# Performance work log

Measured on AMD Instinct MI355X. Metric: run time of the kernel, lower is better.

The kernel has to match this reference:

```python
import jax, jax.numpy as jnp
import numpy as np

B = 65536      # batch
D = 512        # embedding_dim
H = 256        # hidden_size
NB = 6         # num_branch


def setup_inputs() -> dict:
    key = jax.random.key(0)
    ks = jax.random.split(key, 12)
    sc = 0.05
    s = lambda k, shape: (jax.random.normal(k, shape, jnp.float32) * sc)
    inp = {}
    inp["embedding"] = jax.random.normal(ks[0], (B, D), jnp.float32)
    inp["speed"] = jax.random.normal(ks[1], (B,), jnp.float32)
    inp["command"] = jax.random.randint(ks[2], (B,), 1, NB + 1)  # values 1..6
    # speed_in: Linear(1,H) -> ReLU -> Linear(H,D)   (weights stored [in,out])
    inp["sw1"] = s(ks[3], (1, H)); inp["sb1"] = jnp.zeros((H,), jnp.float32)
    inp["sw2"] = s(ks[4], (H, D)); inp["sb2"] = jnp.zeros((D,), jnp.float32)
    # 6 branch MLPs, stacked along leading axis: D->H->H->3, sigmoid
    inp["bw1"] = s(ks[5], (NB, D, H)); inp["bb1"] = jnp.zeros((NB, H), jnp.float32)
    inp["bw2"] = s(ks[6], (NB, H, H)); inp["bb2"] = jnp.zeros((NB, H), jnp.float32)
    inp["bw3"] = s(ks[7], (NB, H, 3)); inp["bb3"] = jnp.zeros((NB, 3), jnp.float32)
    # speed_out: D->H->H->1
    inp["ow1"] = s(ks[8], (D, H)); inp["ob1"] = jnp.zeros((H,), jnp.float32)
    inp["ow2"] = s(ks[9], (H, H)); inp["ob2"] = jnp.zeros((H,), jnp.float32)
    inp["ow3"] = s(ks[10], (H, 1)); inp["ob3"] = jnp.zeros((1,), jnp.float32)
    return inp


def reference(embedding, speed, command,
              sw1, sb1, sw2, sb2,
              bw1, bb1, bw2, bb2, bw3, bb3,
              ow1, ob1, ow2, ob2, ow3, ob3):
    # embedding += speed_in(speed.unsqueeze(1))
    sh = jax.nn.relu(speed[:, None] @ sw1 + sb1)           # [B,H]
    emb = embedding + (sh @ sw2 + sb2)                      # [B,D]

    # all 6 branches computed densely (as in the original), then masked
    h = jax.nn.relu(jnp.einsum('bd,ndh->nbh', emb, bw1) + bb1[:, None, :])   # [NB,B,H]
    h = jax.nn.relu(jnp.einsum('nbh,nhk->nbk', h, bw2) + bb2[:, None, :])    # [NB,B,H]
    br = jax.nn.sigmoid(jnp.einsum('nbh,nho->nbo', h, bw3) + bb3[:, None, :])  # [NB,B,3]

    # mask: branch i selected where i == command - 1
    mask = (jnp.arange(NB)[:, None] == (command - 1)[None, :]).astype(br.dtype)  # [NB,B]
    control_pred = jnp.sum(br * mask[:, :, None], axis=0)   # [B,3]

    # speed_out head
    t = jax.nn.relu(emb @ ow1 + ob1)
    t = jax.nn.relu(t @ ow2 + ob2)
    speed_pred = t @ ow3 + ob3                               # [B,1]
    return control_pred, speed_pred
```

## Files before the change

### kernel.cpp

```cpp
#include <hip/hip_runtime.h>
#include <math.h>


#define B_ 65536
#define D_ 512
#define H_ 256

typedef float  f32x4   __attribute__((ext_vector_type(4)));
typedef __bf16 bf16x8  __attribute__((ext_vector_type(8)));
typedef __bf16 bf16x4  __attribute__((ext_vector_type(4)));
typedef float  float4v __attribute__((ext_vector_type(4)));

#define OFF_PERM     256
#define OFF_PACK     262400
#define WS_NEEDED    3277056

#define PKO_SW2   0u
#define PKO_BW1   131072u
#define PKO_BW2   917504u
#define PKO_OW1   1310720u
#define PKO_OW2   1441792u

#define PITCH_E 520


__global__ __launch_bounds__(256) void k_count(const int* __restrict__ command,
                                               int* __restrict__ counts) {
    __shared__ int lh[6];
    int t = threadIdx.x;
    if (t < 6) lh[t] = 0;
    __syncthreads();
    int i = blockIdx.x * 256 + t;
    int4 v = ((const int4*)command)[i];
    int a[4] = {v.x, v.y, v.z, v.w};
    #pragma unroll
    for (int j = 0; j < 4; ++j) {
        int c = min(max(a[j] - 1, 0), 5);
        atomicAdd(&lh[c], 1);
    }
    __syncthreads();
    if (t < 6) atomicAdd(&counts[t], lh[t]);
}


__global__ __launch_bounds__(256) void k_prepB(const int* __restrict__ command,
                                               const int* __restrict__ counts,
                                               int* __restrict__ cursor2,
                                               int* __restrict__ perm,
                                               const float* __restrict__ sw2,
                                               const float* __restrict__ bw1,
                                               const float* __restrict__ bw2,
                                               const float* __restrict__ ow1,
                                               const float* __restrict__ ow2,
                                               __bf16* __restrict__ PK) {
    int t = threadIdx.x;
    if (blockIdx.x < 256) {
        __shared__ int lh[6], lbase[6];
        if (t < 6) lh[t] = 0;
        __syncthreads();
        int i = blockIdx.x * 256 + t;
        int c = command[i] - 1; c = min(max(c, 0), 5);
        int rank = atomicAdd(&lh[c], 1);
        __syncthreads();
        if (t < 6) {
            int base = 0;
            #pragma unroll
            for (int k = 0; k < 6; ++k) base += (k < t) ? counts[k] : 0;
            lbase[t] = base + atomicAdd(&cursor2[t], lh[t]);
        }
        __syncthreads();
        perm[lbase[c] + rank] = i;
        return;
    }
    int b = blockIdx.x - 256;
    const float* src; int srcN, colOff; unsigned dstOff; int tt;
    if (b < 64)       { int s = b >> 5;        tt = b & 31;  src = sw2;                          srcN = 512; colOff = s * 256; dstOff = PKO_SW2 + s * 65536u; }
    else if (b < 448) { int i = b - 64;  int c = i >> 6; tt = i & 63; src = bw1 + (size_t)c * 512 * 256; srcN = 256; colOff = 0; dstOff = PKO_BW1 + c * 131072u; }
    else if (b < 640) { int i = b - 448; int c = i >> 5; tt = i & 31; src = bw2 + (size_t)c * 256 * 256; srcN = 256; colOff = 0; dstOff = PKO_BW2 + c * 65536u; }
    else if (b < 704) { tt = b - 640; src = ow1; srcN = 256; colOff = 0; dstOff = PKO_OW1; }
    else              { tt = b - 704; src = ow2; srcN = 256; colOff = 0; dstOff = PKO_OW2; }
    int kc = tt >> 2, nt = tt & 3;
    int k0 = kc * 32, n0 = nt * 64;

    __shared__ __bf16 T[64][34];
    #pragma unroll
    for (int p = 0; p < 2; ++p) {
        int idx = p * 256 + t;
        int k = idx >> 4, n4 = idx & 15;
        float4v v = *(const float4v*)(src + (size_t)(k0 + k) * srcN + colOff + n0 + n4 * 4);
        T[n4 * 4 + 0][k] = (__bf16)v[0];
        T[n4 * 4 + 1][k] = (__bf16)v[1];
        T[n4 * 4 + 2][k] = (__bf16)v[2];
        T[n4 * 4 + 3][k] = (__bf16)v[3];
    }
    __syncthreads();
    int n = t >> 2, seg = t & 3;
    bf16x8 v;
    #pragma unroll
    for (int j = 0; j < 8; ++j) v[j] = T[n][seg * 8 + j];
    *(bf16x8*)(PK + dstOff + ((unsigned)(kc * 256 + n0 + n) * 32u + seg * 8u)) = v;
}


__global__ __launch_bounds__(512, 4) void k_fused(
    const float* __restrict__ embedding, const float* __restrict__ speed,
    const int*   __restrict__ command,
    const float* __restrict__ sw1, const float* __restrict__ sb1,
    const float* __restrict__ sb2,
    const float* __restrict__ bb1, const float* __restrict__ bb2,
    const float* __restrict__ bw3, const float* __restrict__ bb3,
    const float* __restrict__ ob1, const float* __restrict__ ob2,
    const float* __restrict__ ow3, const float* __restrict__ ob3,
    const int* __restrict__ perm, const __bf16* __restrict__ PK,
    float* __restrict__ out)
{
    __shared__ __bf16 s_x[64 * PITCH_E];
    __shared__ float  s_head[64][4];
    __shared__ int    s_row[64];
    __shared__ int    s_cmd[64];
    __shared__ float  s_spd[64];

    const int tid = threadIdx.x;
    const int w = tid >> 6, lane = tid & 63;
    const int lm = lane & 15, kg = lane >> 4;
    const int R0 = blockIdx.x * 64;

    if (tid < 64) {
        int r = perm[R0 + tid];
        s_row[tid] = r;
        int c = command[r] - 1; c = min(max(c, 0), 5);
        s_cmd[tid] = c;
        s_spd[tid] = speed[r];
        s_head[tid][0] = 0.f; s_head[tid][1] = 0.f; s_head[tid][2] = 0.f; s_head[tid][3] = 0.f;
    }
    __syncthreads();

    #pragma unroll
    for (int it = 0; it < 16; ++it) {
        int idx = it * 512 + tid;
        int row = idx >> 7, c4 = idx & 127;
        float4v v = __builtin_nontemporal_load(
            (const float4v*)(embedding + (size_t)s_row[row] * D_ + c4 * 4));
        bf16x4 pv;
        pv[0] = (__bf16)v[0]; pv[1] = (__bf16)v[1];
        pv[2] = (__bf16)v[2]; pv[3] = (__bf16)v[3];
        *(bf16x4*)(s_x + row * PITCH_E + c4 * 4) = pv;
    }
    __syncthreads();

    const int cmin = s_cmd[0], cmax = s_cmd[63];

    {
        float spd[4];
        #pragma unroll
        for (int nt = 0; nt < 4; ++nt) spd[nt] = s_spd[nt * 16 + lm];
        const unsigned slice = (unsigned)(w >> 2) * 65536u;
        const int mbase = (w & 3) * 64;
        f32x4 dacc[4][4];
        #pragma unroll
        for (int mt = 0; mt < 4; ++mt)
            #pragma unroll
            for (int nt = 0; nt < 4; ++nt) dacc[mt][nt] = f32x4{0.f, 0.f, 0.f, 0.f};
        #pragma unroll 4
        for (int ks = 0; ks < 8; ++ks) {
            const int k0 = ks * 32 + kg * 8;
            float4v w0 = *(const float4v*)(sw1 + k0);
            float4v w1 = *(const float4v*)(sw1 + k0 + 4);
            float4v c0 = *(const float4v*)(sb1 + k0);
            float4v c1 = *(const float4v*)(sb1 + k0 + 4);
            bf16x8 bns[4];
            #pragma unroll
            for (int nt = 0; nt < 4; ++nt)
                #pragma unroll
                for (int j = 0; j < 4; ++j) {
                    bns[nt][j]     = (__bf16)fmaxf(spd[nt] * w0[j] + c0[j], 0.f);
                    bns[nt][j + 4] = (__bf16)fmaxf(spd[nt] * w1[j] + c1[j], 0.f);
                }
            const __bf16* ap = PK + PKO_SW2 + slice + (size_t)ks * 8192
                             + (size_t)(mbase + lm) * 32 + kg * 8;
            __builtin_amdgcn_s_setprio(1);
            #pragma unroll
            for (int mt = 0; mt < 4; ++mt) {
                bf16x8 av = *(const bf16x8*)(ap + mt * 512);
                #pragma unroll
                for (int nt = 0; nt < 4; ++nt)
                    dacc[mt][nt] = __builtin_amdgcn_mfma_f32_16x16x32_bf16(av, bns[nt], dacc[mt][nt], 0, 0, 0);
            }
            __builtin_amdgcn_s_setprio(0);
        }
        #pragma unroll
        for (int mt = 0; mt < 4; ++mt) {
            int colb = w * 64 + mt * 16 + kg * 4;
            float4v sbv = *(const float4v*)(sb2 + colb);
            #pragma unroll
            for (int nt = 0; nt < 4; ++nt) {
                int row = nt * 16 + lm;
                bf16x4* p = (bf16x4*)(s_x + row * PITCH_E + colb);
                bf16x4 old = *p;
                bf16x4 nv;
                #pragma unroll
                for (int g = 0; g < 4; ++g)
                    nv[g] = (__bf16)(dacc[mt][nt][g] + sbv[g] + (float)old[g]);
                *p = nv;
            }
        }
    }
    __syncthreads();

    const bool roleB = (w < 4);
    const int colbase = (w & 3) * 64;
    const unsigned laneoffB = (unsigned)(colbase + lm) * 32u + kg * 8u;
    const __bf16* aXbase = s_x + lm * PITCH_E + kg * 8;

    bf16x4 res[4][4];
    if (roleB) {
        for (int c = cmin; c <= cmax; ++c) {
            const __bf16* bb = PK + PKO_BW1 + (unsigned)c * 131072u + laneoffB;
            f32x4 ah[4][4];
            #pragma unroll
            for (int mt = 0; mt < 4; ++mt)
                #pragma unroll
                for (int ct = 0; ct < 4; ++ct) ah[mt][ct] = f32x4{0.f, 0.f, 0.f, 0.f};
            #pragma unroll 4
            for (int ks = 0; ks < 16; ++ks) {
                bf16x8 a[4];
                #pragma unroll
                for (int mt = 0; mt < 4; ++mt)
                    a[mt] = *(const bf16x8*)(aXbase + mt * 16 * PITCH_E + ks * 32);
                __builtin_amdgcn_s_setprio(1);
                #pragma unroll
                for (int ct = 0; ct < 4; ++ct) {
                    bf16x8 bv = *(const bf16x8*)(bb + (size_t)ks * 8192 + ct * 512);
                    #pragma unroll
                    for (int mt = 0; mt < 4; ++mt)
                        ah[mt][ct] = __builtin_amdgcn_mfma_f32_16x16x32_bf16(a[mt], bv, ah[mt][ct], 0, 0, 0);
                }
                __builtin_amdgcn_s_setprio(0);
            }
            #pragma unroll
            for (int ct = 0; ct < 4; ++ct) {
                int col = colbase + ct * 16 + lm;
                float b = bb1[c * H_ + col];
                #pragma unroll
                for (int mt = 0; mt < 4; ++mt)
                    #pragma unroll
                    for (int g = 0; g < 4; ++g)
                        if (s_cmd[mt * 16 + kg * 4 + g] == c)
                            res[mt][ct][g] = (__bf16)fmaxf(ah[mt][ct][g] + b, 0.f);
            }
        }
    } else {
        const __bf16* bb = PK + PKO_OW1 + laneoffB;
        f32x4 ta[4][4];
        #pragma unroll
        for (int mt = 0; mt < 4; ++mt)
            #pragma unroll
            for (int ct = 0; ct < 4; ++ct) ta[mt][ct] = f32x4{0.f, 0.f, 0.f, 0.f};
        #pragma unroll 4
        for (int ks = 0; ks < 16; ++ks) {
            bf16x8 a[4];
            #pragma unroll
            for (int mt = 0; mt < 4; ++mt)
                a[mt] = *(const bf16x8*)(aXbase + mt * 16 * PITCH_E + ks * 32);
            __builtin_amdgcn_s_setprio(1);
            #pragma unroll
            for (int ct = 0; ct < 4; ++ct) {
                bf16x8 bv = *(const bf16x8*)(bb + (size_t)ks * 8192 + ct * 512);
                #pragma unroll
                for (int mt = 0; mt < 4; ++mt)
                    ta[mt][ct] = __builtin_amdgcn_mfma_f32_16x16x32_bf16(a[mt], bv, ta[mt][ct], 0, 0, 0);
            }
            __builtin_amdgcn_s_setprio(0);
        }
        #pragma unroll
        for (int ct = 0; ct < 4; ++ct) {
            int col = colbase + ct * 16 + lm;
            float b = ob1[col];
            #pragma unroll
            for (int mt = 0; mt < 4; ++mt)
                #pragma unroll
                for (int g = 0; g < 4; ++g)
                    res[mt][ct][g] = (__bf16)fmaxf(ta[mt][ct][g] + b, 0.f);
        }
    }
    __syncthreads();

    {
        const int colW = (roleB ? 0 : 256) + colbase;
        #pragma unroll
        for (int ct = 0; ct < 4; ++ct) {
            int col = colW + ct * 16 + lm;
            #pragma unroll
            for (int mt = 0; mt < 4; ++mt)
                #pragma unroll
                for (int g = 0; g < 4; ++g)
                    s_x[(mt * 16 + kg * 4 + g) * PITCH_E + col] = res[mt][ct][g];
        }
    }
    __syncthreads();

    const __bf16* aHbase = s_x + lm * PITCH_E + (roleB ? 0 : 256) + kg * 8;
    if (roleB) {
        for (int c = cmin; c <= cmax; ++c) {
            const __bf16* bb = PK + PKO_BW2 + (unsigned)c * 65536u + laneoffB;
            #pragma unroll
            for (int rh = 0; rh < 2; ++rh) {
                f32x4 hh[2][4];
                #pragma unroll
                for (int mt = 0; mt < 2; ++mt)
                    #pragma unroll
                    for (int ct = 0; ct < 4; ++ct) hh[mt][ct] = f32x4{0.f, 0.f, 0.f, 0.f};
                #pragma unroll 4
                for (int ks = 0; ks < 8; ++ks) {
                    bf16x8 a0 = *(const bf16x8*)(aHbase + (rh * 2 + 0) * 16 * PITCH_E + ks * 32);
                    bf16x8 a1 = *(const bf16x8*)(aHbase + (rh * 2 + 1) * 16 * PITCH_E + ks * 32);
                    __builtin_amdgcn_s_setprio(1);
                    #pragma unroll
                    for (int ct = 0; ct < 4; ++ct) {
                        bf16x8 bv = *(const bf16x8*)(bb + (size_t)ks * 8192 + ct * 512);
                        hh[0][ct] = __builtin_amdgcn_mfma_f32_16x16x32_bf16(a0, bv, hh[0][ct], 0, 0, 0);
                        hh[1][ct] = __builtin_amdgcn_mfma_f32_16x16x32_bf16(a1, bv, hh[1][ct], 0, 0, 0);
                    }
                    __builtin_amdgcn_s_setprio(0);
                }
                float ph[2][4][3];
                #pragma unroll
                for (int mt = 0; mt < 2; ++mt)
                    #pragma unroll
                    for (int g = 0; g < 4; ++g) { ph[mt][g][0] = 0.f; ph[mt][g][1] = 0.f; ph[mt][g][2] = 0.f; }
                #pragma unroll
                for (int ct = 0; ct < 4; ++ct) {
                    int col = colbase + ct * 16 + lm;
                    float b  = bb2[c * H_ + col];
                    float w0 = bw3[(c * H_ + col) * 3 + 0];
                    float w1 = bw3[(c * H_ + col) * 3 + 1];
                    float w2 = bw3[(c * H_ + col) * 3 + 2];
                    #pragma unroll
                    for (int mt = 0; mt < 2; ++mt)
                        #pragma unroll
                        for (int g = 0; g < 4; ++g) {
                            float h = fmaxf(hh[mt][ct][g] + b, 0.f);
                            ph[mt][g][0] += h * w0; ph[mt][g][1] += h * w1; ph[mt][g][2] += h * w2;
                        }
                }
                #pragma unroll
                for (int mt = 0; mt < 2; ++mt)
                    #pragma unroll
                    for (int g = 0; g < 4; ++g)
                        #pragma unroll
                        for (int o = 0; o < 3; ++o) {
                            float v = ph[mt][g][o];
                            v += __shfl_xor(v, 1); v += __shfl_xor(v, 2);
                            v += __shfl_xor(v, 4); v += __shfl_xor(v, 8);
                            ph[mt][g][o] = v;
                        }
                if (lm == 0) {
                    #pragma unroll
                    for (int mt = 0; mt < 2; ++mt)
                        #pragma unroll
                        for (int g = 0; g < 4; ++g) {
                            int row = (rh * 2 + mt) * 16 + kg * 4 + g;
                            if (s_cmd[row] == c) {
                                atomicAdd(&s_head[row][0], ph[mt][g][0]);
                                atomicAdd(&s_head[row][1], ph[mt][g][1]);
                                atomicAdd(&s_head[row][2], ph[mt][g][2]);
                            }
                        }
                }
            }
        }
    } else {
        float sp[4][4];
        #pragma unroll
        for (int mt = 0; mt < 4; ++mt)
            #pragma unroll
            for (int g = 0; g < 4; ++g) sp[mt][g] = 0.f;
        const __bf16* bb = PK + PKO_OW2 + laneoffB;
        #pragma unroll
        for (int rh = 0; rh < 2; ++rh) {
            f32x4 hh[2][4];
            #pragma unroll
            for (int mt = 0; mt < 2; ++mt)
                #pragma unroll
                for (int ct = 0; ct < 4; ++ct) hh[mt][ct] = f32x4{0.f, 0.f, 0.f, 0.f};
            #pragma unroll 4
            for (int ks = 0; ks < 8; ++ks) {
                bf16x8 a0 = *(const bf16x8*)(aHbase + (rh * 2 + 0) * 16 * PITCH_E + ks * 32);
                bf16x8 a1 = *(const bf16x8*)(aHbase + (rh * 2 + 1) * 16 * PITCH_E + ks * 32);
                __builtin_amdgcn_s_setprio(1);
                #pragma unroll
                for (int ct = 0; ct < 4; ++ct) {
                    bf16x8 bv = *(const bf16x8*)(bb + (size_t)ks * 8192 + ct * 512);
                    hh[0][ct] = __builtin_amdgcn_mfma_f32_16x16x32_bf16(a0, bv, hh[0][ct], 0, 0, 0);
                    hh[1][ct] = __builtin_amdgcn_mfma_f32_16x16x32_bf16(a1, bv, hh[1][ct], 0, 0, 0);
                }
                __builtin_amdgcn_s_setprio(0);
            }
            #pragma unroll
            for (int ct = 0; ct < 4; ++ct) {
                int col = colbase + ct * 16 + lm;
                float b = ob2[col], wv = ow3[col];
                #pragma unroll
                for (int mt = 0; mt < 2; ++mt)
                    #pragma unroll
                    for (int g = 0; g < 4; ++g)
                        sp[rh * 2 + mt][g] += fmaxf(hh[mt][ct][g] + b, 0.f) * wv;
            }
        }
        #pragma unroll
        for (int mt = 0; mt < 4; ++mt)
            #pragma unroll
            for (int g = 0; g < 4; ++g) {
                float v = sp[mt][g];
                v += __shfl_xor(v, 1); v += __shfl_xor(v, 2);
                v += __shfl_xor(v, 4); v += __shfl_xor(v, 8);
                if (lm == 0) atomicAdd(&s_head[mt * 16 + kg * 4 + g][3], v);
            }
    }
    __syncthreads();

    if (tid < 64) {
        int r = s_row[tid], c = s_cmd[tid];
        #pragma unroll
        for (int o = 0; o < 3; ++o) {
            float x = s_head[tid][o] + bb3[c * 3 + o];
            __builtin_nontemporal_store(1.f / (1.f + __expf(-x)), &out[(size_t)r * 3 + o]);
        }
        __builtin_nontemporal_store(s_head[tid][3] + ob3[0], &out[(size_t)3 * B_ + r]);
    }
}


__global__ __launch_bounds__(256) void cilrs_slow(
    const float* __restrict__ embedding, const float* __restrict__ speed,
    const int* __restrict__ command,
    const float* __restrict__ sw1, const float* __restrict__ sb1,
    const float* __restrict__ sw2, const float* __restrict__ sb2,
    const float* __restrict__ bw1, const float* __restrict__ bb1,
    const float* __restrict__ bw2, const float* __restrict__ bb2,
    const float* __restrict__ bw3, const float* __restrict__ bb3,
    const float* __restrict__ ow1, const float* __restrict__ ob1,
    const float* __restrict__ ow2, const float* __restrict__ ob2,
    const float* __restrict__ ow3, const float* __restrict__ ob3,
    float* __restrict__ out)
{
    const int row = blockIdx.x;
    const int j   = threadIdx.x;
    __shared__ float sh[H_];
    __shared__ float emb[D_];
    __shared__ float h1[H_];
    __shared__ float h2[H_];
    const float spd = speed[row];
    { float v = spd * sw1[j] + sb1[j]; sh[j] = v > 0.f ? v : 0.f; }
    __syncthreads();
    {
        float a0 = 0.f, a1 = 0.f;
        for (int h = 0; h < H_; ++h) {
            const float s = sh[h];
            a0 += s * sw2[h * D_ + j];
            a1 += s * sw2[h * D_ + j + 256];
        }
        emb[j]       = embedding[(size_t)row * D_ + j]       + a0 + sb2[j];
        emb[j + 256] = embedding[(size_t)row * D_ + j + 256] + a1 + sb2[j + 256];
    }
    __syncthreads();
    const int n = command[row] - 1;
    {
        const float* wp = bw1 + (size_t)n * D_ * H_;
        float a = 0.f;
        for (int d = 0; d < D_; ++d) a += emb[d] * wp[d * H_ + j];
        a += bb1[n * H_ + j];
        h1[j] = a > 0.f ? a : 0.f;
    }
    __syncthreads();
    {
        const float* wp = bw2 + (size_t)n * H_ * H_;
        float a = 0.f;
        for (int h = 0; h < H_; ++h) a += h1[h] * wp[h * H_ + j];
        a += bb2[n * H_ + j];
        h2[j] = a > 0.f ? a : 0.f;
    }
    __syncthreads();
    {
        float a = 0.f;
        for (int d = 0; d < D_; ++d) a += emb[d] * ow1[d * H_ + j];
        a += ob1[j];
        sh[j] = a > 0.f ? a : 0.f;
    }
    __syncthreads();
    {
        float a = 0.f;
        for (int h = 0; h < H_; ++h) a += sh[h] * ow2[h * H_ + j];
        a += ob2[j];
        h1[j] = a > 0.f ? a : 0.f;
    }
    __syncthreads();
    if (j < 3) {
        const float* wp = bw3 + (size_t)n * H_ * 3;
        float a = 0.f;
        for (int h = 0; h < H_; ++h) a += h2[h] * wp[h * 3 + j];
        a += bb3[n * 3 + j];
        out[(size_t)row * 3 + j] = 1.f / (1.f + expf(-a));
    } else if (j == 3) {
        float a = 0.f;
        for (int h = 0; h < H_; ++h) a += h1[h] * ow3[h];
        a += ob3[0];
        out[(size_t)B_ * 3 + row] = a;
    }
}


extern "C" void kernel_launch(void* const* d_in, const int* in_sizes, int n_in,
                              void* d_out, int out_size, void* d_ws, size_t ws_size,
                              hipStream_t stream) {
    const float* embedding = (const float*)d_in[0];
    const float* speed     = (const float*)d_in[1];
    const int*   command   = (const int*)  d_in[2];
    const float* sw1 = (const float*)d_in[3];
    const float* sb1 = (const float*)d_in[4];
    const float* sw2 = (const float*)d_in[5];
    const float* sb2 = (const float*)d_in[6];
    const float* bw1 = (const float*)d_in[7];
    const float* bb1 = (const float*)d_in[8];
    const float* bw2 = (const float*)d_in[9];
    const float* bb2 = (const float*)d_in[10];
    const float* bw3 = (const float*)d_in[11];
    const float* bb3 = (const float*)d_in[12];
    const float* ow1 = (const float*)d_in[13];
    const float* ob1 = (const float*)d_in[14];
    const float* ow2 = (const float*)d_in[15];
    const float* ob2 = (const float*)d_in[16];
    const float* ow3 = (const float*)d_in[17];
    const float* ob3 = (const float*)d_in[18];
    float* out = (float*)d_out;

    if (ws_size < (size_t)WS_NEEDED) {
        cilrs_slow<<<B_, 256, 0, stream>>>(embedding, speed, command,
                                           sw1, sb1, sw2, sb2,
                                           bw1, bb1, bw2, bb2, bw3, bb3,
                                           ow1, ob1, ow2, ob2, ow3, ob3, out);
        return;
    }

    char* ws = (char*)d_ws;
    int*    counts  = (int*)    ws;
    int*    cursor2 = (int*)   (ws + 24);
    int*    perm    = (int*)   (ws + OFF_PERM);
    __bf16* PK      = (__bf16*)(ws + OFF_PACK);

    hipMemsetAsync(ws, 0, 64, stream);
    k_count<<<64, 256, 0, stream>>>(command, counts);
    k_prepB<<<992, 256, 0, stream>>>(command, counts, cursor2, perm,
                                     sw2, bw1, bw2, ow1, ow2, PK);
    k_fused<<<B_ / 64, 512, 0, stream>>>(embedding, speed, command,
                                         sw1, sb1, sb2,
                                         bb1, bb2, bw3, bb3,
                                         ob1, ob2, ow3, ob3,
                                         perm, PK, out);
}
```

Baseline: 351.5 us.

## Double rows per block to 128 and reshape per-wave MFMA tiles

The fused kernel now handles 128 rows per block with 1024 threads instead of 64 rows with 512. Each wave computes 32 output columns over all 128 rows rather than 64 columns over 64 rows, and every layer's MFMA loops are reshaped to match. Each weight fragment fetched from global memory now feeds twice as many rows, which targets L2 weight traffic. In exchange, the LDS footprint roughly doubles, likely allowing only one block per CU. A 128-row block may also span more branch commands, which adds redundant branch work.

```diff
diff --git a/kernel.cpp b/kernel.cpp
--- a/kernel.cpp
+++ b/kernel.cpp
@@ -102,7 +102,7 @@
 }
 
 
-__global__ __launch_bounds__(512, 4) void k_fused(
+__global__ __launch_bounds__(1024, 4) void k_fused(
     const float* __restrict__ embedding, const float* __restrict__ speed,
     const int*   __restrict__ command,
     const float* __restrict__ sw1, const float* __restrict__ sb1,
@@ -114,18 +114,18 @@
     const int* __restrict__ perm, const __bf16* __restrict__ PK,
     float* __restrict__ out)
 {
-    __shared__ __bf16 s_x[64 * PITCH_E];
-    __shared__ float  s_head[64][4];
-    __shared__ int    s_row[64];
-    __shared__ int    s_cmd[64];
-    __shared__ float  s_spd[64];
+    __shared__ __bf16 s_x[128 * PITCH_E];
+    __shared__ float  s_head[128][4];
+    __shared__ int    s_row[128];
+    __shared__ int    s_cmd[128];
+    __shared__ float  s_spd[128];
 
     const int tid = threadIdx.x;
     const int w = tid >> 6, lane = tid & 63;
     const int lm = lane & 15, kg = lane >> 4;
-    const int R0 = blockIdx.x * 64;
-
-    if (tid < 64) {
+    const int R0 = blockIdx.x * 128;
+
+    if (tid < 128) {
         int r = perm[R0 + tid];
         s_row[tid] = r;
         int c = command[r] - 1; c = min(max(c, 0), 5);
@@ -137,7 +137,7 @@
 
     #pragma unroll
     for (int it = 0; it < 16; ++it) {
-        int idx = it * 512 + tid;
+        int idx = it * 1024 + tid;
         int row = idx >> 7, c4 = idx & 127;
         float4v v = __builtin_nontemporal_load(
             (const float4v*)(embedding + (size_t)s_row[row] * D_ + c4 * 4));
@@ -148,101 +148,105 @@
     }
     __syncthreads();
 
-    const int cmin = s_cmd[0], cmax = s_cmd[63];
-
-    {
-        float spd[4];
-        #pragma unroll
-        for (int nt = 0; nt < 4; ++nt) spd[nt] = s_spd[nt * 16 + lm];
-        const unsigned slice = (unsigned)(w >> 2) * 65536u;
-        const int mbase = (w & 3) * 64;
-        f32x4 dacc[4][4];
-        #pragma unroll
-        for (int mt = 0; mt < 4; ++mt)
-            #pragma unroll
-            for (int nt = 0; nt < 4; ++nt) dacc[mt][nt] = f32x4{0.f, 0.f, 0.f, 0.f};
-        #pragma unroll 4
-        for (int ks = 0; ks < 8; ++ks) {
-            const int k0 = ks * 32 + kg * 8;
-            float4v w0 = *(const float4v*)(sw1 + k0);
-            float4v w1 = *(const float4v*)(sw1 + k0 + 4);
-            float4v c0 = *(const float4v*)(sb1 + k0);
-            float4v c1 = *(const float4v*)(sb1 + k0 + 4);
-            bf16x8 bns[4];
-            #pragma unroll
-            for (int nt = 0; nt < 4; ++nt)
-                #pragma unroll
-                for (int j = 0; j < 4; ++j) {
-                    bns[nt][j]     = (__bf16)fmaxf(spd[nt] * w0[j] + c0[j], 0.f);
-                    bns[nt][j + 4] = (__bf16)fmaxf(spd[nt] * w1[j] + c1[j], 0.f);
-                }
-            const __bf16* ap = PK + PKO_SW2 + slice + (size_t)ks * 8192
-                             + (size_t)(mbase + lm) * 32 + kg * 8;
-            __builtin_amdgcn_s_setprio(1);
-            #pragma unroll
-            for (int mt = 0; mt < 4; ++mt) {
-                bf16x8 av = *(const bf16x8*)(ap + mt * 512);
+    const int cmin = s_cmd[0], cmax = s_cmd[127];
+
+    {
+        const unsigned slice = (unsigned)(w >> 3) * 65536u;
+        const int mbase = (w & 7) * 32;
+        #pragma unroll
+        for (int p = 0; p < 2; ++p) {
+            float spd[4];
+            #pragma unroll
+            for (int nt = 0; nt < 4; ++nt) spd[nt] = s_spd[p * 64 + nt * 16 + lm];
+            f32x4 dacc[2][4];
+            #pragma unroll
+            for (int mt = 0; mt < 2; ++mt)
+                #pragma unroll
+                for (int nt = 0; nt < 4; ++nt) dacc[mt][nt] = f32x4{0.f, 0.f, 0.f, 0.f};
+            #pragma unroll 2
+            for (int ks = 0; ks < 8; ++ks) {
+                const int k0 = ks * 32 + kg * 8;
+                float4v w0 = *(const float4v*)(sw1 + k0);
+                float4v w1 = *(const float4v*)(sw1 + k0 + 4);
+                float4v c0 = *(const float4v*)(sb1 + k0);
+                float4v c1 = *(const float4v*)(sb1 + k0 + 4);
+                bf16x8 bns[4];
                 #pragma unroll
                 for (int nt = 0; nt < 4; ++nt)
-                    dacc[mt][nt] = __builtin_amdgcn_mfma_f32_16x16x32_bf16(av, bns[nt], dacc[mt][nt], 0, 0, 0);
-            }
-            __builtin_amdgcn_s_setprio(0);
-        }
-        #pragma unroll
-        for (int mt = 0; mt < 4; ++mt) {
-            int colb = w * 64 + mt * 16 + kg * 4;
-            float4v sbv = *(const float4v*)(sb2 + colb);
-            #pragma unroll
-            for (int nt = 0; nt < 4; ++nt) {
-                int row = nt * 16 + lm;
-                bf16x4* p = (bf16x4*)(s_x + row * PITCH_E + colb);
-                bf16x4 old = *p;
-                bf16x4 nv;
-                #pragma unroll
-                for (int g = 0; g < 4; ++g)
-                    nv[g] = (__bf16)(dacc[mt][nt][g] + sbv[g] + (float)old[g]);
-                *p = nv;
-            }
-        }
-    }
-    __syncthreads();
-
-    const bool roleB = (w < 4);
-    const int colbase = (w & 3) * 64;
+                    #pragma unroll
+                    for (int j = 0; j < 4; ++j) {
+                        bns[nt][j]     = (__bf16)fmaxf(spd[nt] * w0[j] + c0[j], 0.f);
+                        bns[nt][j + 4] = (__bf16)fmaxf(spd[nt] * w1[j] + c1[j], 0.f);
+                    }
+                const __bf16* ap = PK + PKO_SW2 + slice + (size_t)ks * 8192
+                                 + (size_t)(mbase + lm) * 32 + kg * 8;
+                __builtin_amdgcn_s_setprio(1);
+                #pragma unroll
+                for (int mt = 0; mt < 2; ++mt) {
+                    bf16x8 av = *(const bf16x8*)(ap + mt * 512);
+                    #pragma unroll
+                    for (int nt = 0; nt < 4; ++nt)
+                        dacc[mt][nt] = __builtin_amdgcn_mfma_f32_16x16x32_bf16(av, bns[nt], dacc[mt][nt], 0, 0, 0);
+                }
+                __builtin_amdgcn_s_setprio(0);
+            }
+            #pragma unroll
+            for (int mt = 0; mt < 2; ++mt) {
+                int colb = w * 32 + mt * 16 + kg * 4;
+                float4v sbv = *(const float4v*)(sb2 + colb);
+                #pragma unroll
+                for (int nt = 0; nt < 4; ++nt) {
+                    int row = p * 64 + nt * 16 + lm;
+                    bf16x4* ptr = (bf16x4*)(s_x + row * PITCH_E + colb);
+                    bf16x4 old = *ptr;
+                    bf16x4 nv;
+                    #pragma unroll
+                    for (int g = 0; g < 4; ++g)
+                        nv[g] = (__bf16)(dacc[mt][nt][g] + sbv[g] + (float)old[g]);
+                    *ptr = nv;
+                }
+            }
+        }
+    }
+    __syncthreads();
+
+    const bool roleB = (w < 8);
+    const int colbase = (w & 7) * 32;
     const unsigned laneoffB = (unsigned)(colbase + lm) * 32u + kg * 8u;
     const __bf16* aXbase = s_x + lm * PITCH_E + kg * 8;
 
-    bf16x4 res[4][4];
+    bf16x4 res[8][2];
     if (roleB) {
         for (int c = cmin; c <= cmax; ++c) {
             const __bf16* bb = PK + PKO_BW1 + (unsigned)c * 131072u + laneoffB;
-            f32x4 ah[4][4];
-            #pragma unroll
-            for (int mt = 0; mt < 4; ++mt)
-                #pragma unroll
-                for (int ct = 0; ct < 4; ++ct) ah[mt][ct] = f32x4{0.f, 0.f, 0.f, 0.f};
-            #pragma unroll 4
+            f32x4 ah[8][2];
+            #pragma unroll
+            for (int mt = 0; mt < 8; ++mt) {
+                ah[mt][0] = f32x4{0.f, 0.f, 0.f, 0.f};
+                ah[mt][1] = f32x4{0.f, 0.f, 0.f, 0.f};
+            }
+            #pragma unroll 2
             for (int ks = 0; ks < 16; ++ks) {
-                bf16x8 a[4];
-                #pragma unroll
-                for (int mt = 0; mt < 4; ++mt)
-                    a[mt] = *(const bf16x8*)(aXbase + mt * 16 * PITCH_E + ks * 32);
+                bf16x8 bv0 = *(const bf16x8*)(bb + (size_t)ks * 8192);
+                bf16x8 bv1 = *(const bf16x8*)(bb + (size_t)ks * 8192 + 512);
                 __builtin_amdgcn_s_setprio(1);
                 #pragma unroll
-                for (int ct = 0; ct < 4; ++ct) {
-                    bf16x8 bv = *(const bf16x8*)(bb + (size_t)ks * 8192 + ct * 512);
-                    #pragma unroll
-                    for (int mt = 0; mt < 4; ++mt)
-                        ah[mt][ct] = __builtin_amdgcn_mfma_f32_16x16x32_bf16(a[mt], bv, ah[mt][ct], 0, 0, 0);
+                for (int mp = 0; mp < 4; ++mp) {
+                    bf16x8 a0 = *(const bf16x8*)(aXbase + (2 * mp + 0) * 16 * PITCH_E + ks * 32);
+                    bf16x8 a1 = *(const bf16x8*)(aXbase + (2 * mp + 1) * 16 * PITCH_E + ks * 32);
+                    ah[2 * mp + 0][0] = __builtin_amdgcn_mfma_f32_16x16x32_bf16(a0, bv0, ah[2 * mp + 0][0], 0, 0, 0);
+                    ah[2 * mp + 0][1] = __builtin_amdgcn_mfma_f32_16x16x32_bf16(a0, bv1, ah[2 * mp + 0][1], 0, 0, 0);
+                    ah[2 * mp + 1][0] = __builtin_amdgcn_mfma_f32_16x16x32_bf16(a1, bv0, ah[2 * mp + 1][0], 0, 0, 0);
+                    ah[2 * mp + 1][1] = __builtin_amdgcn_mfma_f32_16x16x32_bf16(a1, bv1, ah[2 * mp + 1][1], 0, 0, 0);
                 }
                 __builtin_amdgcn_s_setprio(0);
             }
             #pragma unroll
-            for (int ct = 0; ct < 4; ++ct) {
+            for (int ct = 0; ct < 2; ++ct) {
                 int col = colbase + ct * 16 + lm;
                 float b = bb1[c * H_ + col];
                 #pragma unroll
-                for (int mt = 0; mt < 4; ++mt)
+                for (int mt = 0; mt < 8; ++mt)
                     #pragma unroll
                     for (int g = 0; g < 4; ++g)
                         if (s_cmd[mt * 16 + kg * 4 + g] == c)
@@ -251,33 +255,34 @@
         }
     } else {
         const __bf16* bb = PK + PKO_OW1 + laneoffB;
-        f32x4 ta[4][4];
-        #pragma unroll
-        for (int mt = 0; mt < 4; ++mt)
-            #pragma unroll
-            for (int ct = 0; ct < 4; ++ct) ta[mt][ct] = f32x4{0.f, 0.f, 0.f, 0.f};
-        #pragma unroll 4
+        f32x4 ta[8][2];
+        #pragma unroll
+        for (int mt = 0; mt < 8; ++mt) {
+            ta[mt][0] = f32x4{0.f, 0.f, 0.f, 0.f};
+            ta[mt][1] = f32x4{0.f, 0.f, 0.f, 0.f};
+        }
+        #pragma unroll 2
         for (int ks = 0; ks < 16; ++ks) {
-            bf16x8 a[4];
-            #pragma unroll
-            for (int mt = 0; mt < 4; ++mt)
-                a[mt] = *(const bf16x8*)(aXbase + mt * 16 * PITCH_E + ks * 32);
+            bf16x8 bv0 = *(const bf16x8*)(bb + (size_t)ks * 8192);
+            bf16x8 bv1 = *(const bf16x8*)(bb + (size_t)ks * 8192 + 512);
             __builtin_amdgcn_s_setprio(1);
             #pragma unroll
-            for (int ct = 0; ct < 4; ++ct) {
-                bf16x8 bv = *(const bf16x8*)(bb + (size_t)ks * 8192 + ct * 512);
-                #pragma unroll
-                for (int mt = 0; mt < 4; ++mt)
-                    ta[mt][ct] = __builtin_amdgcn_mfma_f32_16x16x32_bf16(a[mt], bv, ta[mt][ct], 0, 0, 0);
+            for (int mp = 0; mp < 4; ++mp) {
+                bf16x8 a0 = *(const bf16x8*)(aXbase + (2 * mp + 0) * 16 * PITCH_E + ks * 32);
+                bf16x8 a1 = *(const bf16x8*)(aXbase + (2 * mp + 1) * 16 * PITCH_E + ks * 32);
+                ta[2 * mp + 0][0] = __builtin_amdgcn_mfma_f32_16x16x32_bf16(a0, bv0, ta[2 * mp + 0][0], 0, 0, 0);
+                ta[2 * mp + 0][1] = __builtin_amdgcn_mfma_f32_16x16x32_bf16(a0, bv1, ta[2 * mp + 0][1], 0, 0, 0);
+                ta[2 * mp + 1][0] = __builtin_amdgcn_mfma_f32_16x16x32_bf16(a1, bv0, ta[2 * mp + 1][0], 0, 0, 0);
+                ta[2 * mp + 1][1] = __builtin_amdgcn_mfma_f32_16x16x32_bf16(a1, bv1, ta[2 * mp + 1][1], 0, 0, 0);
             }
             __builtin_amdgcn_s_setprio(0);
         }
         #pragma unroll
-        for (int ct = 0; ct < 4; ++ct) {
+        for (int ct = 0; ct < 2; ++ct) {
             int col = colbase + ct * 16 + lm;
             float b = ob1[col];
             #pragma unroll
-            for (int mt = 0; mt < 4; ++mt)
+            for (int mt = 0; mt < 8; ++mt)
                 #pragma unroll
                 for (int g = 0; g < 4; ++g)
                     res[mt][ct][g] = (__bf16)fmaxf(ta[mt][ct][g] + b, 0.f);
@@ -288,10 +293,10 @@
     {
         const int colW = (roleB ? 0 : 256) + colbase;
         #pragma unroll
-        for (int ct = 0; ct < 4; ++ct) {
+        for (int ct = 0; ct < 2; ++ct) {
             int col = colW + ct * 16 + lm;
             #pragma unroll
-            for (int mt = 0; mt < 4; ++mt)
+            for (int mt = 0; mt < 8; ++mt)
                 #pragma unroll
                 for (int g = 0; g < 4; ++g)
                     s_x[(mt * 16 + kg * 4 + g) * PITCH_E + col] = res[mt][ct][g];
@@ -305,38 +310,39 @@
             const __bf16* bb = PK + PKO_BW2 + (unsigned)c * 65536u + laneoffB;
             #pragma unroll
             for (int rh = 0; rh < 2; ++rh) {
-                f32x4 hh[2][4];
-                #pragma unroll
-                for (int mt = 0; mt < 2; ++mt)
-                    #pragma unroll
-                    for (int ct = 0; ct < 4; ++ct) hh[mt][ct] = f32x4{0.f, 0.f, 0.f, 0.f};
-                #pragma unroll 4
+                f32x4 hh[4][2];
+                #pragma unroll
+                for (int mt = 0; mt < 4; ++mt) {
+                    hh[mt][0] = f32x4{0.f, 0.f, 0.f, 0.f};
+                    hh[mt][1] = f32x4{0.f, 0.f, 0.f, 0.f};
+                }
+                #pragma unroll 2
                 for (int ks = 0; ks < 8; ++ks) {
-                    bf16x8 a0 = *(const bf16x8*)(aHbase + (rh * 2 + 0) * 16 * PITCH_E + ks * 32);
-                    bf16x8 a1 = *(const bf16x8*)(aHbase + (rh * 2 + 1) * 16 * PITCH_E + ks * 32);
+                    bf16x8 bv0 = *(const bf16x8*)(bb + (size_t)ks * 8192);
+                    bf16x8 bv1 = *(const bf16x8*)(bb + (size_t)ks * 8192 + 512);
                     __builtin_amdgcn_s_setprio(1);
                     #pragma unroll
-                    for (int ct = 0; ct < 4; ++ct) {
-                        bf16x8 bv = *(const bf16x8*)(bb + (size_t)ks * 8192 + ct * 512);
-                        hh[0][ct] = __builtin_amdgcn_mfma_f32_16x16x32_bf16(a0, bv, hh[0][ct], 0, 0, 0);
-                        hh[1][ct] = __builtin_amdgcn_mfma_f32_16x16x32_bf16(a1, bv, hh[1][ct], 0, 0, 0);
+                    for (int mt = 0; mt < 4; ++mt) {
+                        bf16x8 a = *(const bf16x8*)(aHbase + (rh * 4 + mt) * 16 * PITCH_E + ks * 32);
+                        hh[mt][0] = __builtin_amdgcn_mfma_f32_16x16x32_bf16(a, bv0, hh[mt][0], 0, 0, 0);
+                        hh[mt][1] = __builtin_amdgcn_mfma_f32_16x16x32_bf16(a, bv1, hh[mt][1], 0, 0, 0);
                     }
                     __builtin_amdgcn_s_setprio(0);
                 }
-                float ph[2][4][3];
-                #pragma unroll
-                for (int mt = 0; mt < 2; ++mt)
+                float ph[4][4][3];
+                #pragma unroll
+                for (int mt = 0; mt < 4; ++mt)
                     #pragma unroll
                     for (int g = 0; g < 4; ++g) { ph[mt][g][0] = 0.f; ph[mt][g][1] = 0.f; ph[mt][g][2] = 0.f; }
                 #pragma unroll
-                for (int ct = 0; ct < 4; ++ct) {
+                for (int ct = 0; ct < 2; ++ct) {
                     int col = colbase + ct * 16 + lm;
                     float b  = bb2[c * H_ + col];
                     float w0 = bw3[(c * H_ + col) * 3 + 0];
                     float w1 = bw3[(c * H_ + col) * 3 + 1];
                     float w2 = bw3[(c * H_ + col) * 3 + 2];
                     #pragma unroll
-                    for (int mt = 0; mt < 2; ++mt)
+                    for (int mt = 0; mt < 4; ++mt)
                         #pragma unroll
                         for (int g = 0; g < 4; ++g) {
                             float h = fmaxf(hh[mt][ct][g] + b, 0.f);
@@ -344,7 +350,7 @@
                         }
                 }
                 #pragma unroll
-                for (int mt = 0; mt < 2; ++mt)
+                for (int mt = 0; mt < 4; ++mt)
                     #pragma unroll
                     for (int g = 0; g < 4; ++g)
                         #pragma unroll
@@ -356,10 +362,10 @@
                         }
                 if (lm == 0) {
                     #pragma unroll
-                    for (int mt = 0; mt < 2; ++mt)
+                    for (int mt = 0; mt < 4; ++mt)
                         #pragma unroll
                         for (int g = 0; g < 4; ++g) {
-                            int row = (rh * 2 + mt) * 16 + kg * 4 + g;
+                            int row = (rh * 4 + mt) * 16 + kg * 4 + g;
                             if (s_cmd[row] == c) {
                                 atomicAdd(&s_head[row][0], ph[mt][g][0]);
                                 atomicAdd(&s_head[row][1], ph[mt][g][1]);
@@ -370,45 +376,46 @@
             }
         }
     } else {
-        float sp[4][4];
-        #pragma unroll
-        for (int mt = 0; mt < 4; ++mt)
+        float sp[8][4];
+        #pragma unroll
+        for (int mt = 0; mt < 8; ++mt)
             #pragma unroll
             for (int g = 0; g < 4; ++g) sp[mt][g] = 0.f;
         const __bf16* bb = PK + PKO_OW2 + laneoffB;
         #pragma unroll
         for (int rh = 0; rh < 2; ++rh) {
-            f32x4 hh[2][4];
-            #pragma unroll
-            for (int mt = 0; mt < 2; ++mt)
-                #pragma unroll
-                for (int ct = 0; ct < 4; ++ct) hh[mt][ct] = f32x4{0.f, 0.f, 0.f, 0.f};
-            #pragma unroll 4
+            f32x4 hh[4][2];
+            #pragma unroll
+            for (int mt = 0; mt < 4; ++mt) {
+                hh[mt][0] = f32x4{0.f, 0.f, 0.f, 0.f};
+                hh[mt][1] = f32x4{0.f, 0.f, 0.f, 0.f};
+            }
+            #pragma unroll 2
             for (int ks = 0; ks < 8; ++ks) {
-                bf16x8 a0 = *(const bf16x8*)(aHbase + (rh * 2 + 0) * 16 * PITCH_E + ks * 32);
-                bf16x8 a1 = *(const bf16x8*)(aHbase + (rh * 2 + 1) * 16 * PITCH_E + ks * 32);
+                bf16x8 bv0 = *(const bf16x8*)(bb + (size_t)ks * 8192);
+                bf16x8 bv1 = *(const bf16x8*)(bb + (size_t)ks * 8192 + 512);
                 __builtin_amdgcn_s_setprio(1);
                 #pragma unroll
-                for (int ct = 0; ct < 4; ++ct) {
-                    bf16x8 bv = *(const bf16x8*)(bb + (size_t)ks * 8192 + ct * 512);
-                    hh[0][ct] = __builtin_amdgcn_mfma_f32_16x16x32_bf16(a0, bv, hh[0][ct], 0, 0, 0);
-                    hh[1][ct] = __builtin_amdgcn_mfma_f32_16x16x32_bf16(a1, bv, hh[1][ct], 0, 0, 0);
+                for (int mt = 0; mt < 4; ++mt) {
+                    bf16x8 a = *(const bf16x8*)(aHbase + (rh * 4 + mt) * 16 * PITCH_E + ks * 32);
+                    hh[mt][0] = __builtin_amdgcn_mfma_f32_16x16x32_bf16(a, bv0, hh[mt][0], 0, 0, 0);
+                    hh[mt][1] = __builtin_amdgcn_mfma_f32_16x16x32_bf16(a, bv1, hh[mt][1], 0, 0, 0);
                 }
                 __builtin_amdgcn_s_setprio(0);
             }
             #pragma unroll
-            for (int ct = 0; ct < 4; ++ct) {
+            for (int ct = 0; ct < 2; ++ct) {
                 int col = colbase + ct * 16 + lm;
                 float b = ob2[col], wv = ow3[col];
                 #pragma unroll
-                for (int mt = 0; mt < 2; ++mt)
+                for (int mt = 0; mt < 4; ++mt)
                     #pragma unroll
                     for (int g = 0; g < 4; ++g)
-                        sp[rh * 2 + mt][g] += fmaxf(hh[mt][ct][g] + b, 0.f) * wv;
-            }
-        }
-        #pragma unroll
-        for (int mt = 0; mt < 4; ++mt)
+                        sp[rh * 4 + mt][g] += fmaxf(hh[mt][ct][g] + b, 0.f) * wv;
+            }
+        }
+        #pragma unroll
+        for (int mt = 0; mt < 8; ++mt)
             #pragma unroll
             for (int g = 0; g < 4; ++g) {
                 float v = sp[mt][g];
@@ -419,7 +426,7 @@
     }
     __syncthreads();
 
-    if (tid < 64) {
+    if (tid < 128) {
         int r = s_row[tid], c = s_cmd[tid];
         #pragma unroll
         for (int o = 0; o < 3; ++o) {
@@ -552,9 +559,9 @@
     k_count<<<64, 256, 0, stream>>>(command, counts);
     k_prepB<<<992, 256, 0, stream>>>(command, counts, cursor2, perm,
                                      sw2, bw1, bw2, ow1, ow2, PK);
-    k_fused<<<B_ / 64, 512, 0, stream>>>(embedding, speed, command,
-                                         sw1, sb1, sb2,
-                                         bb1, bb2, bw3, bb3,
-                                         ob1, ob2, ow3, ob3,
-                                         perm, PK, out);
+    k_fused<<<B_ / 128, 1024, 0, stream>>>(embedding, speed, command,
+                                           sw1, sb1, sb2,
+                                           bb1, bb2, bw3, bb3,
+                                           ob1, ob2, ow3, ob3,
+                                           perm, PK, out);
 }
```

After: 374.2 us. 1.06x slower.
